# Kernel optimization log

Measured on AMD Instinct MI355X. Metric: run time of the kernel, lower is better.

Reference implementation:

```python
import jax, jax.numpy as jnp
import numpy as np
from jax import lax

N_NODES = 100000
D = 2048
E = 8192
H = 128
SIM_THRESHOLD = 0.7
EPS = 1e-8  # torch CosineSimilarity default eps


def setup_inputs() -> dict:
    key = jax.random.key(0)
    ks = jax.random.split(key, 8)
    x_idx = jax.random.randint(ks[0], (E,), 0, N_NODES, dtype=jnp.int32)
    y_idx = jax.random.randint(ks[1], (E,), 0, N_NODES, dtype=jnp.int32)
    x_feat = jax.random.normal(ks[2], (E, D), dtype=jnp.float32)
    y_feat = jax.random.normal(ks[3], (E, D), dtype=jnp.float32)
    # make ~half the pairs highly similar so the sim >= 0.7 branch is exercised
    coin = jax.random.uniform(ks[4], (E, 1)) < 0.5
    y_feat = jnp.where(coin, x_feat + 0.5 * y_feat, y_feat)
    W1 = 0.02 * jax.random.normal(ks[5], (H, 2 * D), dtype=jnp.float32)
    b1 = jnp.zeros((H,), jnp.float32)
    W2 = 0.02 * jax.random.normal(ks[6], (1, H), dtype=jnp.float32)
    b2 = jnp.zeros((1,), jnp.float32)
    parent = jnp.arange(N_NODES, dtype=jnp.int32)
    rank = jnp.ones((N_NODES,), jnp.float32)
    return {"x_idx": x_idx, "y_idx": y_idx, "x_feat": x_feat, "y_feat": y_feat,
            "W1": W1, "b1": b1, "W2": W2, "b2": b2,
            "parent": parent, "rank": rank}


def _gate(x_feat, y_feat, W1, b1, W2, b2):
    # cosine similarity with torch's eps clamp on each norm
    dot = jnp.sum(x_feat * y_feat, axis=-1)
    nx = jnp.maximum(jnp.sqrt(jnp.sum(x_feat * x_feat, axis=-1)), EPS)
    ny = jnp.maximum(jnp.sqrt(jnp.sum(y_feat * y_feat, axis=-1)), EPS)
    sim = dot / (nx * ny)
    h = jax.nn.relu(jnp.concatenate([x_feat, y_feat], axis=-1) @ W1.T + b1)  # [E, H]
    attn = jax.nn.sigmoid(h @ W2.T + b2)[:, 0]                               # [E]
    mask = sim >= SIM_THRESHOLD
    w = jnp.where(mask, attn, jnp.zeros_like(attn))
    return w, mask


def _find_root(parent, i):
    # iterative root find
    root = lax.while_loop(lambda r: parent[r] != r, lambda r: parent[r], i)
    # path compression: point every node on the path at root (matches recursive torch find)
    def comp_body(state):
        p, j = state
        nj = p[j]
        p = p.at[j].set(root)
        return p, nj
    parent, _ = lax.while_loop(lambda s: s[1] != root, comp_body, (parent, i))
    return parent, root


def reference(x_idx, y_idx, x_feat, y_feat, W1, b1, W2, b2, parent, rank):
    w, mask = _gate(x_feat, y_feat, W1, b1, W2, b2)

    def step(carry, inp):
        x, y, wi, m = inp
        def do(c):
            p, r = c
            p, rx = _find_root(p, x)
            p, ry = _find_root(p, y)
            bigger_x = r[rx] > r[ry]
            big = jnp.where(bigger_x, rx, ry)
            small = jnp.where(bigger_x, ry, rx)
            same = rx == ry
            # if roots are equal: no structural change, no rank update
            p = p.at[jnp.where(same, big, small)].set(big)
            r = r.at[big].add(jnp.where(same, 0.0, r[small] * wi))
            return p, r
        carry = lax.cond(m, do, lambda c: c, carry)
        return carry, None

    (parent, rank), _ = lax.scan(step, (parent, rank), (x_idx, y_idx, w, mask))
    return w, parent, rank
```

## Files before the change

### kernel.cpp

```cpp
#include <hip/hip_runtime.h>
#include <math.h>

#define E_EDGES 8192
#define D_FEAT 2048
#define K2 4096
#define H_DIM 128
#define N_NODES 100000
#define SIM_TH 0.7f
#define NSLOTS (2 * E_EDGES)
#define GBM 16

__global__ __launch_bounds__(256) void sim_kernel(const float* __restrict__ xf,
                                                  const float* __restrict__ yf,
                                                  float* __restrict__ sim) {
    int gid  = blockIdx.x * blockDim.x + threadIdx.x;
    int wave = gid >> 6;
    int lane = threadIdx.x & 63;
    if (wave >= E_EDGES) return;
    const float4* xp = (const float4*)(xf + (size_t)wave * D_FEAT);
    const float4* yp = (const float4*)(yf + (size_t)wave * D_FEAT);
    float dot = 0.f, xx = 0.f, yy = 0.f;
#pragma unroll
    for (int j = 0; j < 8; ++j) {
        float4 a = xp[lane + j * 64];
        float4 b = yp[lane + j * 64];
        dot += a.x * b.x + a.y * b.y + a.z * b.z + a.w * b.w;
        xx  += a.x * a.x + a.y * a.y + a.z * a.z + a.w * a.w;
        yy  += b.x * b.x + b.y * b.y + b.z * b.z + b.w * b.w;
    }
#pragma unroll
    for (int off = 32; off; off >>= 1) {
        dot += __shfl_xor(dot, off);
        xx  += __shfl_xor(xx, off);
        yy  += __shfl_xor(yy, off);
    }
    if (lane == 0) {
        float nx = fmaxf(sqrtf(xx), 1e-8f);
        float ny = fmaxf(sqrtf(yy), 1e-8f);
        sim[wave] = dot / (nx * ny);
    }
}

__global__ void initmap_kernel(int* __restrict__ fo, int* __restrict__ orig,
                               float* __restrict__ wout) {
    int i = blockIdx.x * blockDim.x + threadIdx.x;
    if (i < N_NODES) fo[i] = 0x7FFFFFFF;
    if (i < NSLOTS)  orig[i] = -1;
    if (i < E_EDGES) wout[i] = 0.f;
}

__global__ void claim_kernel(const int* __restrict__ x_idx, const int* __restrict__ y_idx,
                             int* __restrict__ fo) {
    int i = blockIdx.x * blockDim.x + threadIdx.x;
    if (i >= NSLOTS) return;
    int e = i >> 1;
    int v = (i & 1) ? y_idx[e] : x_idx[e];
    atomicMin(&fo[v], i);
}

__global__ void orig_kernel(const int* __restrict__ x_idx, const int* __restrict__ y_idx,
                            const int* __restrict__ fo, int* __restrict__ orig) {
    int i = blockIdx.x * blockDim.x + threadIdx.x;
    if (i >= NSLOTS) return;
    int e = i >> 1;
    int v = (i & 1) ? y_idx[e] : x_idx[e];
    if (fo[v] == i) orig[i] = v;
}

__global__ __launch_bounds__(256) void maskscan_kernel(
        const int* __restrict__ x_idx, const int* __restrict__ y_idx,
        const int* __restrict__ fo, const float* __restrict__ sim,
        int4* __restrict__ rec, int* __restrict__ nmask) {
    __shared__ int partial[256];
    int t = threadIdx.x;
    int cnt = 0;
    for (int j = 0; j < 32; ++j) {
        int e = t * 32 + j;
        cnt += (sim[e] >= SIM_TH) ? 1 : 0;
    }
    partial[t] = cnt;
    __syncthreads();
    for (int off = 1; off < 256; off <<= 1) {
        int mine  = partial[t];
        int other = (t >= off) ? partial[t - off] : 0;
        __syncthreads();
        partial[t] = mine + other;
        __syncthreads();
    }
    int pos = partial[t] - cnt;
    if (t == 255) {
        int nn = partial[255];
        *nmask = nn;
        for (int j = 0; j < 4; ++j) rec[nn + j] = make_int4(0, 0, 0, 0);
    }
    for (int j = 0; j < 32; ++j) {
        int e = t * 32 + j;
        if (sim[e] >= SIM_TH) {
            int4 r;
            r.x = fo[x_idx[e]];
            r.y = fo[y_idx[e]];
            r.z = e;
            r.w = 0;
            rec[pos++] = r;
        }
    }
}

__global__ __launch_bounds__(256) void gate_kernel(
        const float* __restrict__ xf, const float* __restrict__ yf,
        const float* __restrict__ W1, const float* __restrict__ b1,
        const float* __restrict__ W2, const float* __restrict__ b2,
        int4* __restrict__ rec, const int* __restrict__ nmask,
        float* __restrict__ wout) {
    __shared__ float As[2][GBM][32];
    __shared__ float Bs[2][H_DIM][33];
    __shared__ float hbuf[GBM][132];
    __shared__ int   elds[GBM];

    int n  = *nmask;
    int b0 = blockIdx.x * GBM;
    if (b0 >= n) return;

    int t = threadIdx.x;
    if (t < GBM) {
        int idx = b0 + t;
        elds[t] = (idx < n) ? rec[idx].z : rec[b0].z;
    }
    __syncthreads();

    const int  arow = t >> 3;
    const int  acol = (t & 7) * 4;
    const bool aact = (t < 128);
    const int  brow = t >> 3;
    const int  bcol = (t & 7) * 4;

    const float* xrow = xf + (size_t)elds[aact ? arow : 0] * D_FEAT + acol;
    const float* yrow = yf + (size_t)elds[aact ? arow : 0] * D_FEAT + acol;
    const float* w1p0 = W1 + (size_t)(brow +  0) * K2 + bcol;
    const float* w1p1 = W1 + (size_t)(brow + 32) * K2 + bcol;
    const float* w1p2 = W1 + (size_t)(brow + 64) * K2 + bcol;
    const float* w1p3 = W1 + (size_t)(brow + 96) * K2 + bcol;

    float4 aR = make_float4(0.f, 0.f, 0.f, 0.f);
    float4 bR0, bR1, bR2, bR3;

    if (aact) aR = *(const float4*)(xrow + 0);
    bR0 = *(const float4*)(w1p0 + 0);
    bR1 = *(const float4*)(w1p1 + 0);
    bR2 = *(const float4*)(w1p2 + 0);
    bR3 = *(const float4*)(w1p3 + 0);
    if (aact) *(float4*)(&As[0][arow][acol]) = aR;
    Bs[0][brow +  0][bcol + 0] = bR0.x; Bs[0][brow +  0][bcol + 1] = bR0.y;
    Bs[0][brow +  0][bcol + 2] = bR0.z; Bs[0][brow +  0][bcol + 3] = bR0.w;
    Bs[0][brow + 32][bcol + 0] = bR1.x; Bs[0][brow + 32][bcol + 1] = bR1.y;
    Bs[0][brow + 32][bcol + 2] = bR1.z; Bs[0][brow + 32][bcol + 3] = bR1.w;
    Bs[0][brow + 64][bcol + 0] = bR2.x; Bs[0][brow + 64][bcol + 1] = bR2.y;
    Bs[0][brow + 64][bcol + 2] = bR2.z; Bs[0][brow + 64][bcol + 3] = bR2.w;
    Bs[0][brow + 96][bcol + 0] = bR3.x; Bs[0][brow + 96][bcol + 1] = bR3.y;
    Bs[0][brow + 96][bcol + 2] = bR3.z; Bs[0][brow + 96][bcol + 3] = bR3.w;
    __syncthreads();

    const int eb = (t >> 6) * 4;
    const int ln = t & 63;
    float acc[4][2] = {{0.f,0.f},{0.f,0.f},{0.f,0.f},{0.f,0.f}};

    const int NT = K2 / 32;
    for (int tile = 0; tile < NT; ++tile) {
        const int buf = tile & 1;
        if (tile + 1 < NT) {
            int k0 = (tile + 1) * 32;
            if (aact) {
                const float* ap = (k0 < D_FEAT) ? (xrow + k0) : (yrow + (k0 - D_FEAT));
                aR = *(const float4*)ap;
            }
            bR0 = *(const float4*)(w1p0 + k0);
            bR1 = *(const float4*)(w1p1 + k0);
            bR2 = *(const float4*)(w1p2 + k0);
            bR3 = *(const float4*)(w1p3 + k0);
        }
#pragma unroll
        for (int kk = 0; kk < 32; kk += 4) {
            float4 a0 = *(const float4*)(&As[buf][eb + 0][kk]);
            float4 a1 = *(const float4*)(&As[buf][eb + 1][kk]);
            float4 a2 = *(const float4*)(&As[buf][eb + 2][kk]);
            float4 a3 = *(const float4*)(&As[buf][eb + 3][kk]);
            float bl0 = Bs[buf][ln][kk + 0];
            float bl1 = Bs[buf][ln][kk + 1];
            float bl2 = Bs[buf][ln][kk + 2];
            float bl3 = Bs[buf][ln][kk + 3];
            float bh0 = Bs[buf][ln + 64][kk + 0];
            float bh1 = Bs[buf][ln + 64][kk + 1];
            float bh2 = Bs[buf][ln + 64][kk + 2];
            float bh3 = Bs[buf][ln + 64][kk + 3];
            acc[0][0] = fmaf(a0.x, bl0, acc[0][0]);
            acc[0][0] = fmaf(a0.y, bl1, acc[0][0]);
            acc[0][0] = fmaf(a0.z, bl2, acc[0][0]);
            acc[0][0] = fmaf(a0.w, bl3, acc[0][0]);
            acc[0][1] = fmaf(a0.x, bh0, acc[0][1]);
            acc[0][1] = fmaf(a0.y, bh1, acc[0][1]);
            acc[0][1] = fmaf(a0.z, bh2, acc[0][1]);
            acc[0][1] = fmaf(a0.w, bh3, acc[0][1]);
            acc[1][0] = fmaf(a1.x, bl0, acc[1][0]);
            acc[1][0] = fmaf(a1.y, bl1, acc[1][0]);
            acc[1][0] = fmaf(a1.z, bl2, acc[1][0]);
            acc[1][0] = fmaf(a1.w, bl3, acc[1][0]);
            acc[1][1] = fmaf(a1.x, bh0, acc[1][1]);
            acc[1][1] = fmaf(a1.y, bh1, acc[1][1]);
            acc[1][1] = fmaf(a1.z, bh2, acc[1][1]);
            acc[1][1] = fmaf(a1.w, bh3, acc[1][1]);
            acc[2][0] = fmaf(a2.x, bl0, acc[2][0]);
            acc[2][0] = fmaf(a2.y, bl1, acc[2][0]);
            acc[2][0] = fmaf(a2.z, bl2, acc[2][0]);
            acc[2][0] = fmaf(a2.w, bl3, acc[2][0]);
            acc[2][1] = fmaf(a2.x, bh0, acc[2][1]);
            acc[2][1] = fmaf(a2.y, bh1, acc[2][1]);
            acc[2][1] = fmaf(a2.z, bh2, acc[2][1]);
            acc[2][1] = fmaf(a2.w, bh3, acc[2][1]);
            acc[3][0] = fmaf(a3.x, bl0, acc[3][0]);
            acc[3][0] = fmaf(a3.y, bl1, acc[3][0]);
            acc[3][0] = fmaf(a3.z, bl2, acc[3][0]);
            acc[3][0] = fmaf(a3.w, bl3, acc[3][0]);
            acc[3][1] = fmaf(a3.x, bh0, acc[3][1]);
            acc[3][1] = fmaf(a3.y, bh1, acc[3][1]);
            acc[3][1] = fmaf(a3.z, bh2, acc[3][1]);
            acc[3][1] = fmaf(a3.w, bh3, acc[3][1]);
        }
        if (tile + 1 < NT) {
            const int nb = buf ^ 1;
            if (aact) *(float4*)(&As[nb][arow][acol]) = aR;
            Bs[nb][brow +  0][bcol + 0] = bR0.x; Bs[nb][brow +  0][bcol + 1] = bR0.y;
            Bs[nb][brow +  0][bcol + 2] = bR0.z; Bs[nb][brow +  0][bcol + 3] = bR0.w;
            Bs[nb][brow + 32][bcol + 0] = bR1.x; Bs[nb][brow + 32][bcol + 1] = bR1.y;
            Bs[nb][brow + 32][bcol + 2] = bR1.z; Bs[nb][brow + 32][bcol + 3] = bR1.w;
            Bs[nb][brow + 64][bcol + 0] = bR2.x; Bs[nb][brow + 64][bcol + 1] = bR2.y;
            Bs[nb][brow + 64][bcol + 2] = bR2.z; Bs[nb][brow + 64][bcol + 3] = bR2.w;
            Bs[nb][brow + 96][bcol + 0] = bR3.x; Bs[nb][brow + 96][bcol + 1] = bR3.y;
            Bs[nb][brow + 96][bcol + 2] = bR3.z; Bs[nb][brow + 96][bcol + 3] = bR3.w;
        }
        __syncthreads();
    }

#pragma unroll
    for (int j = 0; j < 4; ++j) {
        hbuf[eb + j][ln]      = fmaxf(acc[j][0] + b1[ln], 0.f);
        hbuf[eb + j][ln + 64] = fmaxf(acc[j][1] + b1[ln + 64], 0.f);
    }
    __syncthreads();
    if (t < GBM && b0 + t < n) {
        float s = 0.f;
        for (int c = 0; c < 32; ++c) {
            float p = 0.f;
#pragma unroll
            for (int q = 0; q < 4; ++q)
                p = fmaf(hbuf[t][4 * c + q], W2[4 * c + q], p);
            s += p;
        }
        float logit = s + b2[0];
        float attn  = 1.f / (1.f + expf(-logit));
        wout[elds[t]] = attn;
        ((int*)&rec[b0 + t])[3] = __float_as_int(attn);
    }
}

__global__ __launch_bounds__(1024) void label_kernel(
        const int4* __restrict__ rec, const int* __restrict__ nmask,
        int* __restrict__ elab) {
    extern __shared__ int L[];
    int t = threadIdx.x;
    int n = *nmask;
    for (int c = t; c < NSLOTS; c += 1024) L[c] = c;
    __syncthreads();
    for (;;) {
        if (t == 0) L[NSLOTS] = 0;
        __syncthreads();
        for (int e = t; e < n; e += 1024) {
            int4 r = rec[e];
            int a = L[r.x], b = L[r.y];
            if (a < b)      { atomicMin(&L[r.y], a); L[NSLOTS] = 1; }
            else if (b < a) { atomicMin(&L[r.x], b); L[NSLOTS] = 1; }
        }
        __syncthreads();
        if (!L[NSLOTS]) break;
        __syncthreads();
        for (int c = t; c < NSLOTS; c += 1024) {
            int q  = L[c];
            int qq = L[q];
            if (qq < q) L[c] = qq;
        }
        __syncthreads();
    }
    __syncthreads();
    for (int e = t; e < n; e += 1024) elab[e] = L[rec[e].x];
}

__global__ __launch_bounds__(1024) void radix_kernel(
        int4* __restrict__ bufA, int4* __restrict__ bufB,
        int* __restrict__ keyA, int* __restrict__ keyB,
        const int* __restrict__ nmask,
        int* __restrict__ compStart, int* __restrict__ ncompOut) {
    __shared__ int F[16384];
    __shared__ int P[1024];
    int t = threadIdx.x;
    int n = *nmask;
    int c = (n + 1023) >> 10;

    for (int pass = 0; pass < 4; ++pass) {
        int sh = pass * 4;
        const int4* in   = (pass & 1) ? bufB : bufA;
        int4*       out  = (pass & 1) ? bufA : bufB;
        const int*  kin  = (pass & 1) ? keyB : keyA;
        int*        kout = (pass & 1) ? keyA : keyB;
        for (int q = 0; q < 16; ++q) F[t * 16 + q] = 0;
        __syncthreads();
        for (int j = 0; j < c; ++j) {
            int i = t * c + j;
            if (i < n) {
                int d = (kin[i] >> sh) & 15;
                F[d * 1024 + t] += 1;
            }
        }
        __syncthreads();
        int base = t * 16;
        int loc[16]; int s = 0;
#pragma unroll
        for (int q = 0; q < 16; ++q) { loc[q] = s; s += F[base + q]; }
        P[t] = s;
        __syncthreads();
        for (int off = 1; off < 1024; off <<= 1) {
            int mine  = P[t];
            int other = (t >= off) ? P[t - off] : 0;
            __syncthreads();
            P[t] = mine + other;
            __syncthreads();
        }
        int pre = (t == 0) ? 0 : P[t - 1];
#pragma unroll
        for (int q = 0; q < 16; ++q) F[base + q] = pre + loc[q];
        __syncthreads();
        for (int j = 0; j < c; ++j) {
            int i = t * c + j;
            if (i < n) {
                int k = kin[i];
                int d = (k >> sh) & 15;
                int pos = F[d * 1024 + t]++;
                out[pos]  = in[i];
                kout[pos] = k;
            }
        }
        __syncthreads();
    }

    unsigned char* hd = (unsigned char*)F;
    for (int i = t; i < n; i += 1024) {
        int l  = keyA[i];
        int lp = (i == 0) ? -1 : keyA[i - 1];
        hd[i] = (l != lp) ? 1 : 0;
    }
    __syncthreads();
    int hsum = 0;
    for (int j = 0; j < c; ++j) {
        int i = t * c + j;
        if (i < n) hsum += hd[i];
    }
    P[t] = hsum;
    __syncthreads();
    for (int off = 1; off < 1024; off <<= 1) {
        int mine  = P[t];
        int other = (t >= off) ? P[t - off] : 0;
        __syncthreads();
        P[t] = mine + other;
        __syncthreads();
    }
    int run = P[t] - hsum;
    for (int j = 0; j < c; ++j) {
        int i = t * c + j;
        if (i < n && hd[i]) { compStart[run] = i; ++run; }
    }
    if (t == 1023) { int total = P[1023]; *ncompOut = total; compStart[total] = n; }
}

__global__ __launch_bounds__(1024) void uf_kernel(
        const int4* __restrict__ srec, const int* __restrict__ ncompPtr,
        const int* __restrict__ compStart,
        const int* __restrict__ orig, const float* __restrict__ rin,
        int* __restrict__ gpar, float* __restrict__ grank) {
    extern __shared__ char smem[];
    int2* nd = (int2*)smem;
    int* ndw = (int*)smem;
    int t = threadIdx.x;
    for (int c = t; c < NSLOTS; c += 1024) {
        int o = orig[c];
        float r = (o >= 0) ? rin[o] : 1.0f;
        nd[c] = make_int2(c, __float_as_int(r));
    }
    __syncthreads();

    int ncomp = *ncompPtr;
    for (int c = t; c < ncomp; c += 1024) {
        int s  = compStart[c];
        int en = compStart[c + 1];
        for (int j = s; j < en; ++j) {
            int4 r = srec[j];
            int x = r.x, y = r.y;
            float wi = __int_as_float(r.w);
            int p;
            int rx = x;
            while ((p = ndw[rx * 2]) != rx) rx = p;
            int j2 = x;
            while ((p = ndw[j2 * 2]) != rx) { ndw[j2 * 2] = rx; j2 = p; }
            int ry = y;
            while ((p = ndw[ry * 2]) != ry) ry = p;
            j2 = y;
            while ((p = ndw[j2 * 2]) != ry) { ndw[j2 * 2] = ry; j2 = p; }
            if (rx != ry) {
                float ka = __int_as_float(ndw[rx * 2 + 1]);
                float kb = __int_as_float(ndw[ry * 2 + 1]);
                bool bx = ka > kb;
                int big = bx ? rx : ry, small = bx ? ry : rx;
                float nr = bx ? (ka + kb * wi) : (kb + ka * wi);
                ndw[small * 2]   = big;
                ndw[big * 2 + 1] = __float_as_int(nr);
            }
        }
    }
    __syncthreads();
    for (int c = t; c < NSLOTS; c += 1024) {
        int2 v = nd[c];
        gpar[c] = v.x;
        grank[c] = __int_as_float(v.y);
    }
}

__global__ void finalize_kernel(const int* __restrict__ pin, const float* __restrict__ rin,
                                const int* __restrict__ fo, const int* __restrict__ orig,
                                const int* __restrict__ gpar, const float* __restrict__ grank,
                                float* __restrict__ pout, float* __restrict__ rout) {
    int i = blockIdx.x * blockDim.x + threadIdx.x;
    if (i >= N_NODES) return;
    int c = fo[i];
    float pv, rv;
    if (c != 0x7FFFFFFF) {
        pv = (float)orig[gpar[c]];
        rv = grank[c];
    } else {
        pv = (float)pin[i];
        rv = rin[i];
    }
    pout[i] = pv;
    rout[i] = rv;
}

extern "C" void kernel_launch(void* const* d_in, const int* in_sizes, int n_in,
                              void* d_out, int out_size, void* d_ws, size_t ws_size,
                              hipStream_t stream) {
    const int*   x_idx = (const int*)d_in[0];
    const int*   y_idx = (const int*)d_in[1];
    const float* xf    = (const float*)d_in[2];
    const float* yf    = (const float*)d_in[3];
    const float* W1    = (const float*)d_in[4];
    const float* b1    = (const float*)d_in[5];
    const float* W2    = (const float*)d_in[6];
    const float* b2    = (const float*)d_in[7];
    const int*   pin   = (const int*)d_in[8];
    const float* rin   = (const float*)d_in[9];

    float* out   = (float*)d_out;
    float* w_out = out;
    float* pout  = out + E_EDGES;
    float* rout  = out + E_EDGES + N_NODES;

    char* ws = (char*)d_ws;
    float* sim_ws  = (float*)(ws + 0);
    int*   fo      = (int*)  (ws + 32768);
    int*   orig    = (int*)  (ws + 432768);
    int4*  rec     = (int4*) (ws + 498304);
    int*   nmask   = (int*)  (ws + 629440);
    int*   gpar    = (int*)  (ws + 629504);
    float* grank   = (float*)(ws + 695040);
    int4*  srec    = (int4*) (ws + 760576);
    int*   keyB    = (int*)  (ws + 891648);
    int*   compSt  = (int*)  (ws + 924416);
    int*   ncomp   = (int*)  (ws + 957188);
    int*   keyA    = (int*)sim_ws;

    sim_kernel<<<(E_EDGES * 64) / 256, 256, 0, stream>>>(xf, yf, sim_ws);
    int g = (N_NODES + 255) / 256;
    initmap_kernel<<<g, 256, 0, stream>>>(fo, orig, w_out);
    claim_kernel<<<NSLOTS / 256, 256, 0, stream>>>(x_idx, y_idx, fo);
    orig_kernel<<<NSLOTS / 256, 256, 0, stream>>>(x_idx, y_idx, fo, orig);
    maskscan_kernel<<<1, 256, 0, stream>>>(x_idx, y_idx, fo, sim_ws, rec, nmask);
    gate_kernel<<<E_EDGES / GBM, 256, 0, stream>>>(xf, yf, W1, b1, W2, b2, rec, nmask, w_out);
    label_kernel<<<1, 1024, (NSLOTS + 1) * sizeof(int), stream>>>(rec, nmask, keyA);
    radix_kernel<<<1, 1024, 0, stream>>>(rec, srec, keyA, keyB, nmask, compSt, ncomp);
    uf_kernel<<<1, 1024, 131072, stream>>>(rec, ncomp, compSt, orig, rin, gpar, grank);
    finalize_kernel<<<g, 256, 0, stream>>>(pin, rin, fo, orig, gpar, grank, pout, rout);
}
```

Baseline: 286.4 us.

## Drop LDS tiling in gate GEMM and stream operands directly from global memory

Removes the double-buffered shared-memory staging of feature rows and W1 tiles in the gate kernel, along with the per-tile barriers. Each thread now loads its four edge rows (broadcast across the wave) and its two W1 rows straight from global memory with float4 loads. This takes away the LDS traffic and the synchronisation, but W1 rows are read per lane in a strided, uncoalesced pattern (each lane reads a different 16KB row), so the kernel leans on the cache for reuse.

```diff
diff --git a/kernel.cpp b/kernel.cpp
--- a/kernel.cpp
+++ b/kernel.cpp
@@ -112,8 +112,6 @@
         const float* __restrict__ W2, const float* __restrict__ b2,
         int4* __restrict__ rec, const int* __restrict__ nmask,
         float* __restrict__ wout) {
-    __shared__ float As[2][GBM][32];
-    __shared__ float Bs[2][H_DIM][33];
     __shared__ float hbuf[GBM][132];
     __shared__ int   elds[GBM];
 
@@ -128,117 +126,77 @@
     }
     __syncthreads();
 
-    const int  arow = t >> 3;
-    const int  acol = (t & 7) * 4;
-    const bool aact = (t < 128);
-    const int  brow = t >> 3;
-    const int  bcol = (t & 7) * 4;
-
-    const float* xrow = xf + (size_t)elds[aact ? arow : 0] * D_FEAT + acol;
-    const float* yrow = yf + (size_t)elds[aact ? arow : 0] * D_FEAT + acol;
-    const float* w1p0 = W1 + (size_t)(brow +  0) * K2 + bcol;
-    const float* w1p1 = W1 + (size_t)(brow + 32) * K2 + bcol;
-    const float* w1p2 = W1 + (size_t)(brow + 64) * K2 + bcol;
-    const float* w1p3 = W1 + (size_t)(brow + 96) * K2 + bcol;
-
-    float4 aR = make_float4(0.f, 0.f, 0.f, 0.f);
-    float4 bR0, bR1, bR2, bR3;
-
-    if (aact) aR = *(const float4*)(xrow + 0);
-    bR0 = *(const float4*)(w1p0 + 0);
-    bR1 = *(const float4*)(w1p1 + 0);
-    bR2 = *(const float4*)(w1p2 + 0);
-    bR3 = *(const float4*)(w1p3 + 0);
-    if (aact) *(float4*)(&As[0][arow][acol]) = aR;
-    Bs[0][brow +  0][bcol + 0] = bR0.x; Bs[0][brow +  0][bcol + 1] = bR0.y;
-    Bs[0][brow +  0][bcol + 2] = bR0.z; Bs[0][brow +  0][bcol + 3] = bR0.w;
-    Bs[0][brow + 32][bcol + 0] = bR1.x; Bs[0][brow + 32][bcol + 1] = bR1.y;
-    Bs[0][brow + 32][bcol + 2] = bR1.z; Bs[0][brow + 32][bcol + 3] = bR1.w;
-    Bs[0][brow + 64][bcol + 0] = bR2.x; Bs[0][brow + 64][bcol + 1] = bR2.y;
-    Bs[0][brow + 64][bcol + 2] = bR2.z; Bs[0][brow + 64][bcol + 3] = bR2.w;
-    Bs[0][brow + 96][bcol + 0] = bR3.x; Bs[0][brow + 96][bcol + 1] = bR3.y;
-    Bs[0][brow + 96][bcol + 2] = bR3.z; Bs[0][brow + 96][bcol + 3] = bR3.w;
-    __syncthreads();
-
     const int eb = (t >> 6) * 4;
     const int ln = t & 63;
+
+    const float* x0 = xf + (size_t)elds[eb + 0] * D_FEAT;
+    const float* x1 = xf + (size_t)elds[eb + 1] * D_FEAT;
+    const float* x2 = xf + (size_t)elds[eb + 2] * D_FEAT;
+    const float* x3 = xf + (size_t)elds[eb + 3] * D_FEAT;
+    const float* y0 = yf + (size_t)elds[eb + 0] * D_FEAT;
+    const float* y1 = yf + (size_t)elds[eb + 1] * D_FEAT;
+    const float* y2 = yf + (size_t)elds[eb + 2] * D_FEAT;
+    const float* y3 = yf + (size_t)elds[eb + 3] * D_FEAT;
+    const float* wlo = W1 + (size_t)ln * K2;
+    const float* whi = W1 + (size_t)(ln + 64) * K2;
+
     float acc[4][2] = {{0.f,0.f},{0.f,0.f},{0.f,0.f},{0.f,0.f}};
 
-    const int NT = K2 / 32;
-    for (int tile = 0; tile < NT; ++tile) {
-        const int buf = tile & 1;
-        if (tile + 1 < NT) {
-            int k0 = (tile + 1) * 32;
-            if (aact) {
-                const float* ap = (k0 < D_FEAT) ? (xrow + k0) : (yrow + (k0 - D_FEAT));
-                aR = *(const float4*)ap;
-            }
-            bR0 = *(const float4*)(w1p0 + k0);
-            bR1 = *(const float4*)(w1p1 + k0);
-            bR2 = *(const float4*)(w1p2 + k0);
-            bR3 = *(const float4*)(w1p3 + k0);
-        }
-#pragma unroll
-        for (int kk = 0; kk < 32; kk += 4) {
-            float4 a0 = *(const float4*)(&As[buf][eb + 0][kk]);
-            float4 a1 = *(const float4*)(&As[buf][eb + 1][kk]);
-            float4 a2 = *(const float4*)(&As[buf][eb + 2][kk]);
-            float4 a3 = *(const float4*)(&As[buf][eb + 3][kk]);
-            float bl0 = Bs[buf][ln][kk + 0];
-            float bl1 = Bs[buf][ln][kk + 1];
-            float bl2 = Bs[buf][ln][kk + 2];
-            float bl3 = Bs[buf][ln][kk + 3];
-            float bh0 = Bs[buf][ln + 64][kk + 0];
-            float bh1 = Bs[buf][ln + 64][kk + 1];
-            float bh2 = Bs[buf][ln + 64][kk + 2];
-            float bh3 = Bs[buf][ln + 64][kk + 3];
-            acc[0][0] = fmaf(a0.x, bl0, acc[0][0]);
-            acc[0][0] = fmaf(a0.y, bl1, acc[0][0]);
-            acc[0][0] = fmaf(a0.z, bl2, acc[0][0]);
-            acc[0][0] = fmaf(a0.w, bl3, acc[0][0]);
-            acc[0][1] = fmaf(a0.x, bh0, acc[0][1]);
-            acc[0][1] = fmaf(a0.y, bh1, acc[0][1]);
-            acc[0][1] = fmaf(a0.z, bh2, acc[0][1]);
-            acc[0][1] = fmaf(a0.w, bh3, acc[0][1]);
-            acc[1][0] = fmaf(a1.x, bl0, acc[1][0]);
-            acc[1][0] = fmaf(a1.y, bl1, acc[1][0]);
-            acc[1][0] = fmaf(a1.z, bl2, acc[1][0]);
-            acc[1][0] = fmaf(a1.w, bl3, acc[1][0]);
-            acc[1][1] = fmaf(a1.x, bh0, acc[1][1]);
-            acc[1][1] = fmaf(a1.y, bh1, acc[1][1]);
-            acc[1][1] = fmaf(a1.z, bh2, acc[1][1]);
-            acc[1][1] = fmaf(a1.w, bh3, acc[1][1]);
-            acc[2][0] = fmaf(a2.x, bl0, acc[2][0]);
-            acc[2][0] = fmaf(a2.y, bl1, acc[2][0]);
-            acc[2][0] = fmaf(a2.z, bl2, acc[2][0]);
-            acc[2][0] = fmaf(a2.w, bl3, acc[2][0]);
-            acc[2][1] = fmaf(a2.x, bh0, acc[2][1]);
-            acc[2][1] = fmaf(a2.y, bh1, acc[2][1]);
-            acc[2][1] = fmaf(a2.z, bh2, acc[2][1]);
-            acc[2][1] = fmaf(a2.w, bh3, acc[2][1]);
-            acc[3][0] = fmaf(a3.x, bl0, acc[3][0]);
-            acc[3][0] = fmaf(a3.y, bl1, acc[3][0]);
-            acc[3][0] = fmaf(a3.z, bl2, acc[3][0]);
-            acc[3][0] = fmaf(a3.w, bl3, acc[3][0]);
-            acc[3][1] = fmaf(a3.x, bh0, acc[3][1]);
-            acc[3][1] = fmaf(a3.y, bh1, acc[3][1]);
-            acc[3][1] = fmaf(a3.z, bh2, acc[3][1]);
-            acc[3][1] = fmaf(a3.w, bh3, acc[3][1]);
-        }
-        if (tile + 1 < NT) {
-            const int nb = buf ^ 1;
-            if (aact) *(float4*)(&As[nb][arow][acol]) = aR;
-            Bs[nb][brow +  0][bcol + 0] = bR0.x; Bs[nb][brow +  0][bcol + 1] = bR0.y;
-            Bs[nb][brow +  0][bcol + 2] = bR0.z; Bs[nb][brow +  0][bcol + 3] = bR0.w;
-            Bs[nb][brow + 32][bcol + 0] = bR1.x; Bs[nb][brow + 32][bcol + 1] = bR1.y;
-            Bs[nb][brow + 32][bcol + 2] = bR1.z; Bs[nb][brow + 32][bcol + 3] = bR1.w;
-            Bs[nb][brow + 64][bcol + 0] = bR2.x; Bs[nb][brow + 64][bcol + 1] = bR2.y;
-            Bs[nb][brow + 64][bcol + 2] = bR2.z; Bs[nb][brow + 64][bcol + 3] = bR2.w;
-            Bs[nb][brow + 96][bcol + 0] = bR3.x; Bs[nb][brow + 96][bcol + 1] = bR3.y;
-            Bs[nb][brow + 96][bcol + 2] = bR3.z; Bs[nb][brow + 96][bcol + 3] = bR3.w;
-        }
-        __syncthreads();
-    }
+#define FMA_GROUP(A0, A1, A2, A3, Q, R)                       \
+    acc[0][0] = fmaf(A0.x, Q.x, acc[0][0]);                   \
+    acc[0][0] = fmaf(A0.y, Q.y, acc[0][0]);                   \
+    acc[0][0] = fmaf(A0.z, Q.z, acc[0][0]);                   \
+    acc[0][0] = fmaf(A0.w, Q.w, acc[0][0]);                   \
+    acc[0][1] = fmaf(A0.x, R.x, acc[0][1]);                   \
+    acc[0][1] = fmaf(A0.y, R.y, acc[0][1]);                   \
+    acc[0][1] = fmaf(A0.z, R.z, acc[0][1]);                   \
+    acc[0][1] = fmaf(A0.w, R.w, acc[0][1]);                   \
+    acc[1][0] = fmaf(A1.x, Q.x, acc[1][0]);                   \
+    acc[1][0] = fmaf(A1.y, Q.y, acc[1][0]);                   \
+    acc[1][0] = fmaf(A1.z, Q.z, acc[1][0]);                   \
+    acc[1][0] = fmaf(A1.w, Q.w, acc[1][0]);                   \
+    acc[1][1] = fmaf(A1.x, R.x, acc[1][1]);                   \
+    acc[1][1] = fmaf(A1.y, R.y, acc[1][1]);                   \
+    acc[1][1] = fmaf(A1.z, R.z, acc[1][1]);                   \
+    acc[1][1] = fmaf(A1.w, R.w, acc[1][1]);                   \
+    acc[2][0] = fmaf(A2.x, Q.x, acc[2][0]);                   \
+    acc[2][0] = fmaf(A2.y, Q.y, acc[2][0]);                   \
+    acc[2][0] = fmaf(A2.z, Q.z, acc[2][0]);                   \
+    acc[2][0] = fmaf(A2.w, Q.w, acc[2][0]);                   \
+    acc[2][1] = fmaf(A2.x, R.x, acc[2][1]);                   \
+    acc[2][1] = fmaf(A2.y, R.y, acc[2][1]);                   \
+    acc[2][1] = fmaf(A2.z, R.z, acc[2][1]);                   \
+    acc[2][1] = fmaf(A2.w, R.w, acc[2][1]);                   \
+    acc[3][0] = fmaf(A3.x, Q.x, acc[3][0]);                   \
+    acc[3][0] = fmaf(A3.y, Q.y, acc[3][0]);                   \
+    acc[3][0] = fmaf(A3.z, Q.z, acc[3][0]);                   \
+    acc[3][0] = fmaf(A3.w, Q.w, acc[3][0]);                   \
+    acc[3][1] = fmaf(A3.x, R.x, acc[3][1]);                   \
+    acc[3][1] = fmaf(A3.y, R.y, acc[3][1]);                   \
+    acc[3][1] = fmaf(A3.z, R.z, acc[3][1]);                   \
+    acc[3][1] = fmaf(A3.w, R.w, acc[3][1]);
+
+#pragma unroll 4
+    for (int k = 0; k < D_FEAT; k += 4) {
+        float4 a0 = *(const float4*)(x0 + k);
+        float4 a1 = *(const float4*)(x1 + k);
+        float4 a2 = *(const float4*)(x2 + k);
+        float4 a3 = *(const float4*)(x3 + k);
+        float4 q  = *(const float4*)(wlo + k);
+        float4 r  = *(const float4*)(whi + k);
+        FMA_GROUP(a0, a1, a2, a3, q, r)
+    }
+#pragma unroll 4
+    for (int k = 0; k < D_FEAT; k += 4) {
+        float4 a0 = *(const float4*)(y0 + k);
+        float4 a1 = *(const float4*)(y1 + k);
+        float4 a2 = *(const float4*)(y2 + k);
+        float4 a3 = *(const float4*)(y3 + k);
+        float4 q  = *(const float4*)(wlo + D_FEAT + k);
+        float4 r  = *(const float4*)(whi + D_FEAT + k);
+        FMA_GROUP(a0, a1, a2, a3, q, r)
+    }
+#undef FMA_GROUP
 
 #pragma unroll
     for (int j = 0; j < 4; ++j) {
```

Measured after the change: 516.9 us. 80.5% more time.
